# Kernel tuning notes

Measured on AMD Instinct MI355X. Metric: run time of the kernel, lower is better.

## Reference

```python
import jax, jax.numpy as jnp
import numpy as np

N, D = 12288, 128
T = 0.07  # temperature from __init__ default


def setup_inputs() -> dict:
    key = jax.random.key(0)
    x = jax.random.normal(key, (N, D), dtype=jnp.float32)
    # L2-normalize rows (this loss is defined on unit-norm embeddings;
    # keeps exp(sim / 0.07) finite in fp32 while preserving the exact math).
    x = x / jnp.linalg.norm(x, axis=-1, keepdims=True)
    return {"x": x}


def reference(x):
    # x: [N, D] -> sim: [N, N]
    sim = jnp.matmul(x, x.T) / T
    # faithful to torch: exp -> sum over last dim -> log -> mean (no LSE stabilization)
    return jnp.mean(jnp.log(jnp.sum(jnp.exp(sim), axis=-1)))
```

## Files before the change

### kernel.cpp

```cpp
#include <hip/hip_runtime.h>
#include <hip/hip_bf16.h>

#define NROWS 12288
#define DDIM  128
#define NT    96
#define NTILE 4656
#define NBLK  512
#define MAXT  10

typedef __bf16 bf16x8 __attribute__((ext_vector_type(8)));
typedef float  f32x4  __attribute__((ext_vector_type(4)));

__device__ __forceinline__ unsigned short f2bf(float f) {
    union { float f; unsigned u; } a; a.f = f;
    unsigned r = a.u + 0x7fffu + ((a.u >> 16) & 1u);
    return (unsigned short)(r >> 16);
}

__global__ void convert_kernel(const float* __restrict__ x, unsigned short* __restrict__ xbT,
                               float* __restrict__ rowsum, float* __restrict__ out) {
    int gid = blockIdx.x * 256 + threadIdx.x;
    int e = gid << 3;
    float4 v0 = *(const float4*)(x + e);
    float4 v1 = *(const float4*)(x + e + 4);
    uint4 o;
    o.x = (unsigned)f2bf(v0.x) | ((unsigned)f2bf(v0.y) << 16);
    o.y = (unsigned)f2bf(v0.z) | ((unsigned)f2bf(v0.w) << 16);
    o.z = (unsigned)f2bf(v1.x) | ((unsigned)f2bf(v1.y) << 16);
    o.w = (unsigned)f2bf(v1.z) | ((unsigned)f2bf(v1.w) << 16);
    int r = gid >> 4;
    int c = gid & 15;
    size_t off = ((size_t)((r >> 4) * 4 + (c >> 2)) * 64 + (c & 3) * 16 + (r & 15)) * 8;
    *(uint4*)(xbT + off) = o;
    if (gid < NROWS) rowsum[gid] = 0.f;
    if (gid == 0) out[0] = 0.f;
}

__global__ __launch_bounds__(256, 2) void gemm_exp_rowsum(
    const unsigned short* __restrict__ xbT, float* __restrict__ rowsum)
{
    __shared__ float csumS[MAXT * 128];
    __shared__ int jtArr[MAXT];

    const int tid = threadIdx.x;
    const int g0 = (blockIdx.x * NTILE) >> 9;
    const int g1 = ((blockIdx.x + 1) * NTILE) >> 9;
    const int nt = g1 - g0;

    int bi = 0, rem = g0;
    while (rem >= NT - bi) { rem -= NT - bi; ++bi; }
    int jt = bi + rem;
    const int bi0 = bi, jt0 = jt;

    for (int k = tid; k < MAXT * 128; k += 256) csumS[k] = 0.f;

    const int wave = tid >> 6, lane = tid & 63;
    const int m16 = lane & 15, q = lane >> 4;
    const int wr = wave >> 1, wc = wave & 1;

    bf16x8 af[4][4];
    #define LOAD_AF() do {                                                       \
        _Pragma("unroll")                                                        \
        for (int mi = 0; mi < 4; ++mi) {                                         \
            int arb = bi * 8 + wr * 4 + mi;                                      \
            _Pragma("unroll")                                                    \
            for (int ks = 0; ks < 4; ++ks)                                       \
                af[mi][ks] = *(const bf16x8*)(xbT + ((size_t)(arb * 4 + ks) * 64 + lane) * 8); \
        }                                                                        \
    } while (0)

    LOAD_AF();
    __syncthreads();

    const float SCALE = 20.609929155556625f;

    f32x4 rp4[4];
    #pragma unroll
    for (int mi = 0; mi < 4; ++mi) rp4[mi] = (f32x4){0.f, 0.f, 0.f, 0.f};

    #define FLUSH_RP() do {                                                      \
        _Pragma("unroll")                                                        \
        for (int mi = 0; mi < 4; ++mi) {                                         \
            _Pragma("unroll")                                                    \
            for (int r = 0; r < 4; ++r) {                                        \
                float s = rp4[mi][r];                                            \
                s += __shfl_xor(s, 1);                                           \
                s += __shfl_xor(s, 2);                                           \
                s += __shfl_xor(s, 4);                                           \
                s += __shfl_xor(s, 8);                                           \
                if (m16 == 0)                                                    \
                    atomicAdd(&rowsum[bi * 128 + wr * 64 + mi * 16 + q * 4 + r], s); \
            }                                                                    \
            rp4[mi] = (f32x4){0.f, 0.f, 0.f, 0.f};                               \
        }                                                                        \
    } while (0)

    for (int t = 0; t < nt; ++t) {
        const unsigned short* bbase = xbT + (size_t)((jt * 8 + wc * 4) * 4) * 64 * 8;
        bf16x8 bfr[4][4];
        #pragma unroll
        for (int ks = 0; ks < 4; ++ks)
            #pragma unroll
            for (int ni = 0; ni < 4; ++ni)
                bfr[ks][ni] = *(const bf16x8*)(bbase + ((size_t)(ni * 4 + ks) * 64 + lane) * 8);

        f32x4 acc[4][4] = {};
        #pragma unroll
        for (int ks = 0; ks < 4; ++ks)
            #pragma unroll
            for (int mi = 0; mi < 4; ++mi)
                #pragma unroll
                for (int ni = 0; ni < 4; ++ni)
                    acc[mi][ni] = __builtin_amdgcn_mfma_f32_16x16x32_bf16(
                        af[mi][ks], bfr[ks][ni], acc[mi][ni], 0, 0, 0);

        f32x4 cp4[4];
        #pragma unroll
        for (int ni = 0; ni < 4; ++ni) cp4[ni] = (f32x4){0.f, 0.f, 0.f, 0.f};

        #pragma unroll
        for (int mi = 0; mi < 4; ++mi)
            #pragma unroll
            for (int ni = 0; ni < 4; ++ni) {
                f32x4 sv = acc[mi][ni] * SCALE;
                f32x4 ev;
                ev[0] = __builtin_amdgcn_exp2f(sv[0]);
                ev[1] = __builtin_amdgcn_exp2f(sv[1]);
                ev[2] = __builtin_amdgcn_exp2f(sv[2]);
                ev[3] = __builtin_amdgcn_exp2f(sv[3]);
                rp4[mi] += ev;
                cp4[ni] += ev;
            }

        if (jt != bi) {
            #pragma unroll
            for (int ni = 0; ni < 4; ++ni) {
                float s = (cp4[ni][0] + cp4[ni][1]) + (cp4[ni][2] + cp4[ni][3]);
                s += __shfl_xor(s, 16);
                s += __shfl_xor(s, 32);
                if (q == 0) atomicAdd(&csumS[t * 128 + wc * 64 + ni * 16 + m16], s);
            }
        }

        if (t + 1 < nt) {
            ++jt;
            if (jt == NT) {
                FLUSH_RP();
                ++bi; jt = bi;
                LOAD_AF();
            }
        }
    }
    FLUSH_RP();

    if (tid == 0) {
        int bb = bi0, jj = jt0;
        for (int t = 0; t < nt; ++t) {
            jtArr[t] = jj;
            ++jj; if (jj == NT) { ++bb; jj = bb; }
        }
    }
    __syncthreads();
    for (int k = tid; k < nt * 128; k += 256) {
        float v = csumS[k];
        if (v != 0.f) atomicAdd(&rowsum[jtArr[k >> 7] * 128 + (k & 127)], v);
    }
    #undef LOAD_AF
    #undef FLUSH_RP
}

__global__ void finalize_kernel(const float* __restrict__ rowsum, float* __restrict__ out) {
    __shared__ float red[4];
    int gid = blockIdx.x * 256 + threadIdx.x;
    float lg = __logf(rowsum[gid]);
    #pragma unroll
    for (int off = 1; off < 64; off <<= 1)
        lg += __shfl_xor(lg, off);
    const int wv = threadIdx.x >> 6, ln = threadIdx.x & 63;
    if (ln == 0) red[wv] = lg;
    __syncthreads();
    if (threadIdx.x == 0)
        atomicAdd(out, (red[0] + red[1] + red[2] + red[3]) * (1.0f / (float)NROWS));
}

extern "C" void kernel_launch(void* const* d_in, const int* in_sizes, int n_in,
                              void* d_out, int out_size, void* d_ws, size_t ws_size,
                              hipStream_t stream) {
    const float* x = (const float*)d_in[0];
    float* out = (float*)d_out;

    float* rowsum = (float*)d_ws;
    unsigned short* xbT = (unsigned short*)((char*)d_ws + NROWS * sizeof(float));

    convert_kernel<<<dim3((NROWS * DDIM) / (8 * 256)), dim3(256), 0, stream>>>(x, xbT, rowsum, out);
    gemm_exp_rowsum<<<dim3(NBLK), dim3(256), 0, stream>>>(xbT, rowsum);
    finalize_kernel<<<dim3(NROWS / 256), dim3(256), 0, stream>>>(rowsum, out);
}
```

Measured before the change: 96.63 us.

## Stage A panel in LDS via direct loads and double-buffer B fragments

The A row panel no longer lives in registers. It is copied into shared memory with global_load_lds and read back per k-step inside the compute loop. The B fragments are double-buffered in registers so the next tile's global loads are issued before the current tile's MFMA and exp work, overlapping load latency with compute. This frees registers for the prefetch buffer, at the cost of extra LDS reads per tile and barriers whenever the row block changes.

```diff
diff --git a/kernel.cpp b/kernel.cpp
--- a/kernel.cpp
+++ b/kernel.cpp
@@ -10,6 +10,10 @@
 
 typedef __bf16 bf16x8 __attribute__((ext_vector_type(8)));
 typedef float  f32x4  __attribute__((ext_vector_type(4)));
+
+#define GLD_LDS(g, l) __builtin_amdgcn_global_load_lds(                      \
+    (const __attribute__((address_space(1))) void*)(g),                      \
+    (__attribute__((address_space(3))) void*)(l), 16, 0, 0)
 
 __device__ __forceinline__ unsigned short f2bf(float f) {
     union { float f; unsigned u; } a; a.f = f;
@@ -30,7 +34,7 @@
     o.w = (unsigned)f2bf(v1.z) | ((unsigned)f2bf(v1.w) << 16);
     int r = gid >> 4;
     int c = gid & 15;
-    size_t off = ((size_t)((r >> 4) * 4 + (c >> 2)) * 64 + (c & 3) * 16 + (r & 15)) * 8;
+    int off = (((r >> 4) * 4 + (c >> 2)) * 64 + (c & 3) * 16 + (r & 15)) * 8;
     *(uint4*)(xbT + off) = o;
     if (gid < NROWS) rowsum[gid] = 0.f;
     if (gid == 0) out[0] = 0.f;
@@ -39,6 +43,7 @@
 __global__ __launch_bounds__(256, 2) void gemm_exp_rowsum(
     const unsigned short* __restrict__ xbT, float* __restrict__ rowsum)
 {
+    __shared__ __align__(16) unsigned short Alds[128 * DDIM];
     __shared__ float csumS[MAXT * 128];
     __shared__ int jtArr[MAXT];
 
@@ -58,18 +63,15 @@
     const int m16 = lane & 15, q = lane >> 4;
     const int wr = wave >> 1, wc = wave & 1;
 
-    bf16x8 af[4][4];
-    #define LOAD_AF() do {                                                       \
-        _Pragma("unroll")                                                        \
-        for (int mi = 0; mi < 4; ++mi) {                                         \
-            int arb = bi * 8 + wr * 4 + mi;                                      \
-            _Pragma("unroll")                                                    \
-            for (int ks = 0; ks < 4; ++ks)                                       \
-                af[mi][ks] = *(const bf16x8*)(xbT + ((size_t)(arb * 4 + ks) * 64 + lane) * 8); \
-        }                                                                        \
-    } while (0)
-
-    LOAD_AF();
+    #define STAGE_A() do {                                                       \
+        _Pragma("unroll")                                                        \
+        for (int r8 = 0; r8 < 8; ++r8) {                                         \
+            int ch = r8 * 256 + wave * 64;       \
+            GLD_LDS(xbT + bi * 16384 + (ch + lane) * 8, Alds + ch * 8);          \
+        }                                                                        \
+    } while (0)
+
+    STAGE_A();
     __syncthreads();
 
     const float SCALE = 20.609929155556625f;
@@ -95,68 +97,101 @@
         }                                                                        \
     } while (0)
 
-    for (int t = 0; t < nt; ++t) {
-        const unsigned short* bbase = xbT + (size_t)((jt * 8 + wc * 4) * 4) * 64 * 8;
-        bf16x8 bfr[4][4];
-        #pragma unroll
-        for (int ks = 0; ks < 4; ++ks)
-            #pragma unroll
-            for (int ni = 0; ni < 4; ++ni)
-                bfr[ks][ni] = *(const bf16x8*)(bbase + ((size_t)(ni * 4 + ks) * 64 + lane) * 8);
-
-        f32x4 acc[4][4] = {};
-        #pragma unroll
-        for (int ks = 0; ks < 4; ++ks)
-            #pragma unroll
-            for (int mi = 0; mi < 4; ++mi)
-                #pragma unroll
-                for (int ni = 0; ni < 4; ++ni)
-                    acc[mi][ni] = __builtin_amdgcn_mfma_f32_16x16x32_bf16(
-                        af[mi][ks], bfr[ks][ni], acc[mi][ni], 0, 0, 0);
-
-        f32x4 cp4[4];
-        #pragma unroll
-        for (int ni = 0; ni < 4; ++ni) cp4[ni] = (f32x4){0.f, 0.f, 0.f, 0.f};
-
-        #pragma unroll
-        for (int mi = 0; mi < 4; ++mi)
-            #pragma unroll
-            for (int ni = 0; ni < 4; ++ni) {
-                f32x4 sv = acc[mi][ni] * SCALE;
-                f32x4 ev;
-                ev[0] = __builtin_amdgcn_exp2f(sv[0]);
-                ev[1] = __builtin_amdgcn_exp2f(sv[1]);
-                ev[2] = __builtin_amdgcn_exp2f(sv[2]);
-                ev[3] = __builtin_amdgcn_exp2f(sv[3]);
-                rp4[mi] += ev;
-                cp4[ni] += ev;
-            }
-
-        if (jt != bi) {
-            #pragma unroll
-            for (int ni = 0; ni < 4; ++ni) {
-                float s = (cp4[ni][0] + cp4[ni][1]) + (cp4[ni][2] + cp4[ni][3]);
-                s += __shfl_xor(s, 16);
-                s += __shfl_xor(s, 32);
-                if (q == 0) atomicAdd(&csumS[t * 128 + wc * 64 + ni * 16 + m16], s);
-            }
+    #define LOAD_B(dst, jtv) do {                                                \
+        int bb = ((jtv) * 8 + wc * 4) * 4;                                       \
+        _Pragma("unroll")                                                        \
+        for (int ni = 0; ni < 4; ++ni)                                           \
+            _Pragma("unroll")                                                    \
+            for (int ks = 0; ks < 4; ++ks)                                       \
+                dst[ks][ni] = *(const bf16x8*)(xbT + ((bb + ni * 4 + ks) * 64 + lane) * 8); \
+    } while (0)
+
+    #define COMPUTE(bfr, t) do {                                                 \
+        f32x4 acc[4][4] = {};                                                    \
+        _Pragma("unroll")                                                        \
+        for (int ks = 0; ks < 4; ++ks) {                                         \
+            bf16x8 afk[4];                                                       \
+            _Pragma("unroll")                                                    \
+            for (int mi = 0; mi < 4; ++mi)                                       \
+                afk[mi] = *(const bf16x8*)(&Alds[(((wr * 4 + mi) * 4 + ks) * 64 + lane) * 8]); \
+            _Pragma("unroll")                                                    \
+            for (int mi = 0; mi < 4; ++mi)                                       \
+                _Pragma("unroll")                                                \
+                for (int ni = 0; ni < 4; ++ni)                                   \
+                    acc[mi][ni] = __builtin_amdgcn_mfma_f32_16x16x32_bf16(       \
+                        afk[mi], bfr[ks][ni], acc[mi][ni], 0, 0, 0);             \
+        }                                                                        \
+        f32x4 cp4[4];                                                            \
+        _Pragma("unroll")                                                        \
+        for (int ni = 0; ni < 4; ++ni) cp4[ni] = (f32x4){0.f, 0.f, 0.f, 0.f};    \
+        _Pragma("unroll")                                                        \
+        for (int mi = 0; mi < 4; ++mi)                                           \
+            _Pragma("unroll")                                                    \
+            for (int ni = 0; ni < 4; ++ni) {                                     \
+                f32x4 sv = acc[mi][ni] * SCALE;                                  \
+                f32x4 ev;                                                        \
+                ev[0] = __builtin_amdgcn_exp2f(sv[0]);                           \
+                ev[1] = __builtin_amdgcn_exp2f(sv[1]);                           \
+                ev[2] = __builtin_amdgcn_exp2f(sv[2]);                           \
+                ev[3] = __builtin_amdgcn_exp2f(sv[3]);                           \
+                rp4[mi] += ev;                                                   \
+                cp4[ni] += ev;                                                   \
+            }                                                                    \
+        if (jt != bi) {                                                          \
+            _Pragma("unroll")                                                    \
+            for (int ni = 0; ni < 4; ++ni) {                                     \
+                float s = (cp4[ni][0] + cp4[ni][1]) + (cp4[ni][2] + cp4[ni][3]); \
+                s += __shfl_xor(s, 16);                                          \
+                s += __shfl_xor(s, 32);                                          \
+                if (q == 0) atomicAdd(&csumS[(t) * 128 + wc * 64 + ni * 16 + m16], s); \
+            }                                                                    \
+        }                                                                        \
+    } while (0)
+
+    #define POST(jn, bn, more) do {                                              \
+        if ((more) && (bn) != bi) {                                              \
+            FLUSH_RP();                                                          \
+            bi = (bn);                                                           \
+            __syncthreads();                    \
+            STAGE_A();                                                           \
+            __syncthreads();               \
+        } else {                                                                 \
+            bi = (bn);                                                           \
+        }                                                                        \
+        jt = (jn);                                                               \
+    } while (0)
+
+    bf16x8 bA[4][4], bB[4][4];
+    LOAD_B(bA, jt);
+    int t = 0;
+    for (;;) {
+        {
+            int jn = jt + 1, bn = bi;
+            if (jn == NT) { bn = bi + 1; jn = bn; }
+            bool more = (t + 1 < nt);
+            if (more) LOAD_B(bB, jn);
+            COMPUTE(bA, t);
+            if (!more) break;
+            POST(jn, bn, more);
+            ++t;
         }
-
-        if (t + 1 < nt) {
-            ++jt;
-            if (jt == NT) {
-                FLUSH_RP();
-                ++bi; jt = bi;
-                LOAD_AF();
-            }
+        {
+            int jn = jt + 1, bn = bi;
+            if (jn == NT) { bn = bi + 1; jn = bn; }
+            bool more = (t + 1 < nt);
+            if (more) LOAD_B(bA, jn);
+            COMPUTE(bB, t);
+            if (!more) break;
+            POST(jn, bn, more);
+            ++t;
         }
     }
     FLUSH_RP();
 
     if (tid == 0) {
         int bb = bi0, jj = jt0;
-        for (int t = 0; t < nt; ++t) {
-            jtArr[t] = jj;
+        for (int tt = 0; tt < nt; ++tt) {
+            jtArr[tt] = jj;
             ++jj; if (jj == NT) { ++bb; jj = bb; }
         }
     }
@@ -165,8 +200,11 @@
         float v = csumS[k];
         if (v != 0.f) atomicAdd(&rowsum[jtArr[k >> 7] * 128 + (k & 127)], v);
     }
-    #undef LOAD_AF
+    #undef STAGE_A
     #undef FLUSH_RP
+    #undef LOAD_B
+    #undef COMPUTE
+    #undef POST
 }
 
 __global__ void finalize_kernel(const float* __restrict__ rowsum, float* __restrict__ out) {
```

Measured after the change: 103.0 us. +6.6%, slower.

## Stage A panel in LDS, double-buffer B fragments, raise occupancy

Applied to the files above, without the earlier changes.

The A row-panel fragments move out of registers and into LDS, filled with global_load_lds. The B fragments are now loaded one k-step at a time into two ping-pong register buffers, overlapping loads with MFMA and prefetching the next tile's first k-slice. Freeing those registers lets launch bounds go to 3 waves per SIMD and the grid grow to 768 blocks with fewer tiles each. In exchange, A is re-read from LDS on every k-step, and panel switches need extra block barriers.

```diff
diff --git a/kernel.cpp b/kernel.cpp
--- a/kernel.cpp
+++ b/kernel.cpp
@@ -5,11 +5,15 @@
 #define DDIM  128
 #define NT    96
 #define NTILE 4656
-#define NBLK  512
-#define MAXT  10
+#define NBLK  768
+#define MAXT  7
 
 typedef __bf16 bf16x8 __attribute__((ext_vector_type(8)));
 typedef float  f32x4  __attribute__((ext_vector_type(4)));
+
+#define GLD_LDS(g, l) __builtin_amdgcn_global_load_lds(                      \
+    (const __attribute__((address_space(1))) void*)(g),                      \
+    (__attribute__((address_space(3))) void*)(l), 16, 0, 0)
 
 __device__ __forceinline__ unsigned short f2bf(float f) {
     union { float f; unsigned u; } a; a.f = f;
@@ -30,21 +34,22 @@
     o.w = (unsigned)f2bf(v1.z) | ((unsigned)f2bf(v1.w) << 16);
     int r = gid >> 4;
     int c = gid & 15;
-    size_t off = ((size_t)((r >> 4) * 4 + (c >> 2)) * 64 + (c & 3) * 16 + (r & 15)) * 8;
+    int off = (((r >> 4) * 4 + (c >> 2)) * 64 + (c & 3) * 16 + (r & 15)) * 8;
     *(uint4*)(xbT + off) = o;
     if (gid < NROWS) rowsum[gid] = 0.f;
     if (gid == 0) out[0] = 0.f;
 }
 
-__global__ __launch_bounds__(256, 2) void gemm_exp_rowsum(
+__global__ __launch_bounds__(256, 3) void gemm_exp_rowsum(
     const unsigned short* __restrict__ xbT, float* __restrict__ rowsum)
 {
+    __shared__ __align__(16) unsigned short Alds[128 * DDIM];
     __shared__ float csumS[MAXT * 128];
     __shared__ int jtArr[MAXT];
 
     const int tid = threadIdx.x;
-    const int g0 = (blockIdx.x * NTILE) >> 9;
-    const int g1 = ((blockIdx.x + 1) * NTILE) >> 9;
+    const int g0 = (blockIdx.x * NTILE) / NBLK;
+    const int g1 = ((blockIdx.x + 1) * NTILE) / NBLK;
     const int nt = g1 - g0;
 
     int bi = 0, rem = g0;
@@ -58,18 +63,15 @@
     const int m16 = lane & 15, q = lane >> 4;
     const int wr = wave >> 1, wc = wave & 1;
 
-    bf16x8 af[4][4];
-    #define LOAD_AF() do {                                                       \
-        _Pragma("unroll")                                                        \
-        for (int mi = 0; mi < 4; ++mi) {                                         \
-            int arb = bi * 8 + wr * 4 + mi;                                      \
-            _Pragma("unroll")                                                    \
-            for (int ks = 0; ks < 4; ++ks)                                       \
-                af[mi][ks] = *(const bf16x8*)(xbT + ((size_t)(arb * 4 + ks) * 64 + lane) * 8); \
+    #define STAGE_A() do {                                                       \
+        _Pragma("unroll")                                                        \
+        for (int r8 = 0; r8 < 8; ++r8) {                                         \
+            int ch = r8 * 256 + wave * 64;       \
+            GLD_LDS(xbT + bi * 16384 + (ch + lane) * 8, Alds + ch * 8);          \
         }                                                                        \
     } while (0)
 
-    LOAD_AF();
+    STAGE_A();
     __syncthreads();
 
     const float SCALE = 20.609929155556625f;
@@ -95,24 +97,43 @@
         }                                                                        \
     } while (0)
 
+    #define LOAD_BKS(dst, jtv, ks) do {                                          \
+        int bb = ((jtv) * 8 + wc * 4);                                           \
+        _Pragma("unroll")                                                        \
+        for (int ni = 0; ni < 4; ++ni)                                           \
+            dst[ni] = *(const bf16x8*)(xbT + (((bb + ni) * 4 + (ks)) * 64 + lane) * 8); \
+    } while (0)
+
+    #define MFMA_KS(ks, bfr) do {                                                \
+        bf16x8 afk[4];                                                           \
+        _Pragma("unroll")                                                        \
+        for (int mi = 0; mi < 4; ++mi)                                           \
+            afk[mi] = *(const bf16x8*)(&Alds[(((wr * 4 + mi) * 4 + (ks)) * 64 + lane) * 8]); \
+        _Pragma("unroll")                                                        \
+        for (int mi = 0; mi < 4; ++mi)                                           \
+            _Pragma("unroll")                                                    \
+            for (int ni = 0; ni < 4; ++ni)                                       \
+                acc[mi][ni] = __builtin_amdgcn_mfma_f32_16x16x32_bf16(           \
+                    afk[mi], bfr[ni], acc[mi][ni], 0, 0, 0);                     \
+    } while (0)
+
+    bf16x8 bf0[4], bf1[4];
+    LOAD_BKS(bf0, jt, 0);
+
     for (int t = 0; t < nt; ++t) {
-        const unsigned short* bbase = xbT + (size_t)((jt * 8 + wc * 4) * 4) * 64 * 8;
-        bf16x8 bfr[4][4];
-        #pragma unroll
-        for (int ks = 0; ks < 4; ++ks)
-            #pragma unroll
-            for (int ni = 0; ni < 4; ++ni)
-                bfr[ks][ni] = *(const bf16x8*)(bbase + ((size_t)(ni * 4 + ks) * 64 + lane) * 8);
+        int jn = jt + 1, bn = bi;
+        if (jn == NT) { bn = bi + 1; jn = bn; }
+        const bool more = (t + 1 < nt);
 
         f32x4 acc[4][4] = {};
-        #pragma unroll
-        for (int ks = 0; ks < 4; ++ks)
-            #pragma unroll
-            for (int mi = 0; mi < 4; ++mi)
-                #pragma unroll
-                for (int ni = 0; ni < 4; ++ni)
-                    acc[mi][ni] = __builtin_amdgcn_mfma_f32_16x16x32_bf16(
-                        af[mi][ks], bfr[ks][ni], acc[mi][ni], 0, 0, 0);
+        LOAD_BKS(bf1, jt, 1);
+        MFMA_KS(0, bf0);
+        LOAD_BKS(bf0, jt, 2);
+        MFMA_KS(1, bf1);
+        LOAD_BKS(bf1, jt, 3);
+        MFMA_KS(2, bf0);
+        if (more) LOAD_BKS(bf0, jn, 0);
+        MFMA_KS(3, bf1);
 
         f32x4 cp4[4];
         #pragma unroll
@@ -142,21 +163,21 @@
             }
         }
 
-        if (t + 1 < nt) {
-            ++jt;
-            if (jt == NT) {
-                FLUSH_RP();
-                ++bi; jt = bi;
-                LOAD_AF();
-            }
+        if (more && bn != bi) {
+            FLUSH_RP();
+            bi = bn;
+            __syncthreads();
+            STAGE_A();
+            __syncthreads();
         }
+        jt = jn;
     }
     FLUSH_RP();
 
     if (tid == 0) {
         int bb = bi0, jj = jt0;
-        for (int t = 0; t < nt; ++t) {
-            jtArr[t] = jj;
+        for (int tt = 0; tt < nt; ++tt) {
+            jtArr[tt] = jj;
             ++jj; if (jj == NT) { ++bb; jj = bb; }
         }
     }
@@ -165,8 +186,10 @@
         float v = csumS[k];
         if (v != 0.f) atomicAdd(&rowsum[jtArr[k >> 7] * 128 + (k & 127)], v);
     }
-    #undef LOAD_AF
+    #undef STAGE_A
     #undef FLUSH_RP
+    #undef LOAD_BKS
+    #undef MFMA_KS
 }
 
 __global__ void finalize_kernel(const float* __restrict__ rowsum, float* __restrict__ out) {
```

After: 96.51 us. About the same (-0.1%).
